# Kernel optimization log

Measured on AMD Instinct MI355X. Metric: run time of the kernel, lower is better.

## Reference

```python
import jax, jax.numpy as jnp
import numpy as np

B, C, T, V, K, O = 16, 256, 128, 64, 8, 256


def conv1x1(x, w, b):
    # x: [B,C,T,V], w: [O,C], b: [O] -> [B,O,T,V]
    return jnp.einsum('bctv,oc->botv', x, w) + b[None, :, None, None]


def batchnorm(x, gamma, beta, eps=1e-5):
    # training-mode BatchNorm2d: stats over (B,T,V) per channel
    mean = x.mean(axis=(0, 2, 3), keepdims=True)
    var = x.var(axis=(0, 2, 3), keepdims=True)
    return gamma[None, :, None, None] * (x - mean) * jax.lax.rsqrt(var + eps) + beta[None, :, None, None]


def setup_inputs() -> dict:
    key = jax.random.key(0)
    ks = jax.random.split(key, 16)
    inp = {
        'x': jax.random.normal(ks[0], (B, C, T, V), jnp.float32),
        'A_param': jax.random.normal(ks[1], (1, K, 1, V, V), jnp.float32) * 0.1,
        'alpha': jax.random.normal(ks[2], (), jnp.float32) * 0.1,
        'beta': jax.random.normal(ks[3], (), jnp.float32) * 0.1,
        'w1': jax.random.normal(ks[4], (O, C), jnp.float32) * 0.02,
        'b1': jax.random.normal(ks[5], (O,), jnp.float32) * 0.02,
        'w2': jax.random.normal(ks[6], (O, C), jnp.float32) * 0.02,
        'b2': jax.random.normal(ks[7], (O,), jnp.float32) * 0.02,
        'stem_w': jax.random.normal(ks[8], (O, C), jnp.float32) * 0.02,
        'stem_b': jax.random.normal(ks[9], (O,), jnp.float32) * 0.02,
        'stem_gamma': jnp.ones((O,), jnp.float32),
        'stem_beta': jnp.zeros((O,), jnp.float32),
        'head_w': jax.random.normal(ks[10], (O, O), jnp.float32) * 0.02,
        'head_b': jax.random.normal(ks[11], (O,), jnp.float32) * 0.02,
        'head_gamma': jnp.ones((O,), jnp.float32),
        'head_beta': jnp.zeros((O,), jnp.float32),
    }
    return inp


def reference(x, A_param, alpha, beta, w1, b1, w2, b2,
              stem_w, stem_b, stem_gamma, stem_beta,
              head_w, head_b, head_gamma, head_beta):
    b_, c_, t_, v_ = x.shape
    k_ = A_param.shape[1]
    tp = x.mean(axis=2, keepdims=True)                      # [B,C,1,V]
    x1 = conv1x1(tp, w1, b1).reshape(b_, k_, -1, v_)        # [B,K,c,V]
    x2 = conv1x1(tp, w2, b2).reshape(b_, k_, -1, v_)
    ctr = jnp.tanh(x1[..., :, None] - x2[..., None, :])     # [B,K,c,V,V]
    ada = jax.nn.softmax(jnp.einsum('bkcv,bkcw->bkvw', x1, x2)[:, :, None], axis=-2)  # [B,K,1,V,V]
    A = A_param + ctr * alpha + ada * beta                  # [B,K,c,V,V]
    res = x                                                 # in_channels == out_channels -> Identity
    h = jax.nn.relu(batchnorm(conv1x1(x, stem_w, stem_b), stem_gamma, stem_beta))
    h = h.reshape(b_, k_, -1, t_, v_)                       # [B,K,c,T,V]
    h = jnp.einsum('bkctv,bkcvw->bkctw', h, A).reshape(b_, -1, t_, v_)
    return jax.nn.relu(batchnorm(conv1x1(h, head_w, head_b), head_gamma, head_beta) + res)
```

## Files before the change

kernel.cpp:

```cpp
#include <hip/hip_runtime.h>
#include <cstdint>
#include <cstddef>

#define B_ 16
#define C_ 256
#define T_ 128
#define V_ 64
#define K_ 8
#define O_ 256
#define TN 8192
#define NBT 131072
#define NSL 32

typedef unsigned short ushort_t;
typedef __attribute__((ext_vector_type(8))) short short8;
typedef __attribute__((ext_vector_type(4))) float f32x4;

#define OFF_TP     0
#define OFF_X1     262144
#define OFF_X2     524288
#define OFF_STATS  786432
#define OFF_SSC    819200
#define OFF_HSC    819712
#define OFF_ADA    820224
#define OFF_Z      1344512
#define OFF_H2     34867200

__device__ inline ushort_t f2bf(float f) {
    unsigned u = __builtin_bit_cast(unsigned, f);
    unsigned r = (u + 0x7FFFu + ((u >> 16) & 1u)) >> 16;
    return (ushort_t)r;
}
__device__ inline unsigned pack2(float a, float b) {
    return (unsigned)f2bf(a) | ((unsigned)f2bf(b) << 16);
}
__device__ inline float bf2f_lo(unsigned u) { return __builtin_bit_cast(float, u << 16); }
__device__ inline float bf2f_hi(unsigned u) { return __builtin_bit_cast(float, u & 0xFFFF0000u); }
__device__ inline void gload_lds16(const void* g, void* l) {
    __builtin_amdgcn_global_load_lds((const __attribute__((address_space(1))) unsigned int*)g,
                                     (__attribute__((address_space(3))) unsigned int*)l, 16, 0, 0);
}

__global__ __launch_bounds__(256) void k_xpose2(const float* __restrict__ x,
                                                ushort_t* __restrict__ img,
                                                float* __restrict__ tp) {
    __shared__ float Lt[64][65];
    int tb = blockIdx.x;
    int cg = blockIdx.y;
    int b  = blockIdx.z;
    int tid = threadIdx.x;
    int c0 = cg * 64;
    float4 macc[4] = {};
    for (int tt = 0; tt < 16; tt++) {
        int t = tb * 16 + tt;
        #pragma unroll
        for (int i = 0; i < 4; i++) {
            int e = tid + i * 256;
            int ci = e >> 4, v4 = e & 15;
            float4 v = *(const float4*)(x + ((size_t)(b * C_ + c0 + ci) * 128 + t) * 64 + v4 * 4);
            *(float4*)&Lt[ci][v4 * 4] = v;
            macc[i].x += v.x; macc[i].y += v.y; macc[i].z += v.z; macc[i].w += v.w;
        }
        __syncthreads();
        #pragma unroll
        for (int i = 0; i < 2; i++) {
            int p = tid + i * 256;
            int v = p & 63, qq = (p >> 6) & 3, cc2 = p >> 8;
            int cl0 = cc2 * 32 + qq * 8;
            uint4 u;
            u.x = pack2(Lt[cl0 + 0][v], Lt[cl0 + 1][v]);
            u.y = pack2(Lt[cl0 + 2][v], Lt[cl0 + 3][v]);
            u.z = pack2(Lt[cl0 + 4][v], Lt[cl0 + 5][v]);
            u.w = pack2(Lt[cl0 + 6][v], Lt[cl0 + 7][v]);
            int cc = cg * 2 + cc2;
            size_t dst = ((size_t)(b * 128 + t) * 8 + cc) * 2048 + qq * 512 + v * 8;
            *(uint4*)(img + dst) = u;
        }
        __syncthreads();
    }
    const float r = 1.0f / (float)T_;
    #pragma unroll
    for (int i = 0; i < 4; i++) {
        int e = tid + i * 256;
        int ci = e >> 4, v4 = e & 15;
        float* dst = tp + (size_t)(b * C_ + c0 + ci) * V_ + v4 * 4;
        atomicAdd(&dst[0], macc[i].x * r); atomicAdd(&dst[1], macc[i].y * r);
        atomicAdd(&dst[2], macc[i].z * r); atomicAdd(&dst[3], macc[i].w * r);
    }
}

__global__ __launch_bounds__(256) void k_x1x2a(const float* __restrict__ tp,
                                               const float* __restrict__ w1, const float* __restrict__ b1,
                                               const float* __restrict__ w2, const float* __restrict__ b2,
                                               float* __restrict__ x1, float* __restrict__ x2) {
    int og = blockIdx.x, cc = blockIdx.y, b = blockIdx.z;
    int o  = og * 16 + (threadIdx.x >> 4);
    int v4 = threadIdx.x & 15;
    const float4* ptp = (const float4*)(tp + (size_t)b * C_ * V_) + v4;
    float4 s1 = {0.f,0.f,0.f,0.f}, s2 = {0.f,0.f,0.f,0.f};
    int c0 = cc * 64;
    for (int c = c0; c < c0 + 64; c++) {
        float4 tv = ptp[c * 16];
        float wa = w1[o * C_ + c];
        float wb = w2[o * C_ + c];
        s1.x += tv.x * wa; s1.y += tv.y * wa; s1.z += tv.z * wa; s1.w += tv.w * wa;
        s2.x += tv.x * wb; s2.y += tv.y * wb; s2.z += tv.z * wb; s2.w += tv.w * wb;
    }
    if (cc == 0) {
        float bv1 = b1[o], bv2 = b2[o];
        s1.x += bv1; s1.y += bv1; s1.z += bv1; s1.w += bv1;
        s2.x += bv2; s2.y += bv2; s2.z += bv2; s2.w += bv2;
    }
    float* p1 = x1 + (size_t)(b * O_ + o) * V_ + v4 * 4;
    float* p2 = x2 + (size_t)(b * O_ + o) * V_ + v4 * 4;
    atomicAdd(&p1[0], s1.x); atomicAdd(&p1[1], s1.y); atomicAdd(&p1[2], s1.z); atomicAdd(&p1[3], s1.w);
    atomicAdd(&p2[0], s2.x); atomicAdd(&p2[1], s2.y); atomicAdd(&p2[2], s2.z); atomicAdd(&p2[3], s2.w);
}

__global__ __launch_bounds__(64) void k_ada(const float* __restrict__ x1,
                                            const float* __restrict__ x2,
                                            float* __restrict__ ada) {
    int bid = blockIdx.x;
    int w = bid & 63;
    int k = (bid >> 6) & 7;
    int b = bid >> 9;
    int v = threadIdx.x;
    const float* p1 = x1 + ((size_t)b * O_ + k * 32) * V_;
    const float* p2 = x2 + ((size_t)b * O_ + k * 32) * V_;
    float s = 0.f;
    #pragma unroll
    for (int c = 0; c < 32; c++) s += p1[c * V_ + v] * p2[c * V_ + w];
    float m = s;
    #pragma unroll
    for (int off = 32; off >= 1; off >>= 1) m = fmaxf(m, __shfl_xor(m, off, 64));
    float e = __expf(s - m);
    float sum = e;
    #pragma unroll
    for (int off = 32; off >= 1; off >>= 1) sum += __shfl_xor(sum, off, 64);
    ada[((size_t)(b * K_ + k) * V_ + v) * V_ + w] = e / sum;
}

__global__ __launch_bounds__(256) void k_wconv(const float* __restrict__ w,
                                               ushort_t* __restrict__ img) {
    int flat = blockIdx.x * 256 + threadIdx.x;
    #pragma unroll
    for (int g2 = 0; g2 < 2; g2++) {
        int gi = flat * 2 + g2;
        int cc = gi >> 10;
        int q  = (gi >> 8) & 3;
        int ol = gi & 255;
        int c0 = cc * 32 + q * 8;
        const float* src = w + (size_t)ol * C_ + c0;
        float4 f0 = *(const float4*)src;
        float4 f1 = *(const float4*)(src + 4);
        uint4 u;
        u.x = pack2(f0.x, f0.y); u.y = pack2(f0.z, f0.w);
        u.z = pack2(f1.x, f1.y); u.w = pack2(f1.z, f1.w);
        *(uint4*)(img + (size_t)gi * 8) = u;
    }
}

__global__ __launch_bounds__(256) void k_gemm(const ushort_t* __restrict__ ximg,
                                              const ushort_t* __restrict__ wimg,
                                              const float* __restrict__ bias,
                                              ushort_t* __restrict__ out,
                                              float* __restrict__ psum,
                                              float* __restrict__ psumsq) {
    __shared__ __align__(16) ushort_t sh[2048];
    int tid = threadIdx.x;
    int nblk = blockIdx.x, b = blockIdx.z;
    int wm = tid >> 6;
    int lane = tid & 63, ln = lane & 15, q = lane >> 4;
    f32x4 acc[4][4];
    #pragma unroll
    for (int mt = 0; mt < 4; mt++)
        #pragma unroll
        for (int nt = 0; nt < 4; nt++) acc[mt][nt] = (f32x4){0.f, 0.f, 0.f, 0.f};
    const ushort_t* xbase = ximg + ((size_t)(b * 128 + nblk) * 8) * 2048;
    for (int cc = 0; cc < 8; cc++) {
        gload_lds16(xbase + (size_t)cc * 2048 + wm * 512 + lane * 8, &sh[wm * 512]);
        __syncthreads();
        short8 a[4], bb[4];
        const ushort_t* wc = wimg + (size_t)cc * 8192 + q * 2048;
        #pragma unroll
        for (int mt = 0; mt < 4; mt++)
            a[mt] = *(const short8*)(wc + (wm * 64 + mt * 16 + ln) * 8);
        #pragma unroll
        for (int nt = 0; nt < 4; nt++)
            bb[nt] = *(const short8*)&sh[q * 512 + (nt * 16 + ln) * 8];
        #pragma unroll
        for (int mt = 0; mt < 4; mt++)
            #pragma unroll
            for (int nt = 0; nt < 4; nt++)
                acc[mt][nt] = __builtin_amdgcn_mfma_f32_16x16x32_bf16(a[mt], bb[nt], acc[mt][nt], 0, 0, 0);
        __syncthreads();
    }
    int n_base = nblk * 64;
    int slice = (nblk ^ (b << 3)) & (NSL - 1);
    #pragma unroll
    for (int mt = 0; mt < 4; mt++) {
        int o0 = wm * 64 + mt * 16 + q * 4;
        #pragma unroll
        for (int r = 0; r < 4; r++) {
            float bv = bias[o0 + r];
            float v0 = acc[mt][0][r] + bv, v1 = acc[mt][1][r] + bv;
            float v2 = acc[mt][2][r] + bv, v3 = acc[mt][3][r] + bv;
            ushort_t* orow = out + ((size_t)(b * O_ + o0 + r)) * TN + n_base + ln;
            orow[0] = f2bf(v0); orow[16] = f2bf(v1); orow[32] = f2bf(v2); orow[48] = f2bf(v3);
            float s  = v0 + v1 + v2 + v3;
            float sq = v0 * v0 + v1 * v1 + v2 * v2 + v3 * v3;
            #pragma unroll
            for (int off = 1; off <= 8; off <<= 1) {
                s  += __shfl_xor(s,  off, 64);
                sq += __shfl_xor(sq, off, 64);
            }
            if (ln == 0) {
                atomicAdd(&psum[slice * 256 + o0 + r],   s);
                atomicAdd(&psumsq[slice * 256 + o0 + r], sq);
            }
        }
    }
}

__global__ void k_finalize(const float* __restrict__ psum, const float* __restrict__ psumsq,
                           const float* __restrict__ gamma, const float* __restrict__ betap,
                           float* __restrict__ scale, float* __restrict__ shift) {
    int o = threadIdx.x;
    float s = 0.f, sq = 0.f;
    #pragma unroll
    for (int sl = 0; sl < NSL; sl++) {
        s  += psum[sl * 256 + o];
        sq += psumsq[sl * 256 + o];
    }
    float mean = s  * (1.0f / (float)NBT);
    float var  = sq * (1.0f / (float)NBT) - mean * mean;
    float sc = gamma[o] * rsqrtf(var + 1e-5f);
    scale[o] = sc;
    shift[o] = betap[o] - mean * sc;
}

__global__ __launch_bounds__(256) void k_einsum_mfma(const ushort_t* __restrict__ z,
                                                     const float* __restrict__ x1,
                                                     const float* __restrict__ x2,
                                                     const float* __restrict__ ada,
                                                     const float* __restrict__ A_param,
                                                     const float* __restrict__ alphap,
                                                     const float* __restrict__ betap,
                                                     const float* __restrict__ scale,
                                                     const float* __restrict__ shift,
                                                     ushort_t* __restrict__ h2img) {
    __shared__ float Coms[4096];
    __shared__ float x1s[8][64], x2s[8][64];
    __shared__ __align__(16) ushort_t stg[8192];
    int tid = threadIdx.x;
    int bid = blockIdx.x;
    int mh = bid & 1;
    int q  = (bid >> 1) & 3;
    int k  = (bid >> 3) & 7;
    int b  = bid >> 6;
    int wm = tid >> 6;
    int lane = tid & 63, ln = lane & 15, qq = lane >> 4;
    float alpha = alphap[0], beta = betap[0];

    const float* Apk = A_param + (size_t)k * 4096;
    const float* adk = ada + (size_t)(b * K_ + k) * 4096;
    #pragma unroll
    for (int i = 0; i < 4; i++) {
        int e4 = tid + i * 256;
        float4 ap = *(const float4*)(Apk + (size_t)e4 * 4);
        float4 ad = *(const float4*)(adk + (size_t)e4 * 4);
        float4 cm = {ap.x + beta * ad.x, ap.y + beta * ad.y,
                     ap.z + beta * ad.z, ap.w + beta * ad.w};
        *(float4*)&Coms[e4 * 4] = cm;
    }
    #pragma unroll
    for (int i = 0; i < 2; i++) {
        int e = tid + i * 256;
        int cl = e >> 6, v = e & 63;
        int o1 = k * 32 + q * 8 + cl;
        x1s[cl][v] = x1[((size_t)b * O_ + o1) * V_ + v];
        x2s[cl][v] = x2[((size_t)b * O_ + o1) * V_ + v];
    }
    __syncthreads();

    short8 bfrag[2][2][4];
    #pragma unroll
    for (int half = 0; half < 2; half++) {
        int cl = wm + half * 4;
        #pragma unroll
        for (int kk = 0; kk < 2; kk++) {
            float x1v[8];
            #pragma unroll
            for (int j = 0; j < 8; j++) x1v[j] = x1s[cl][kk * 32 + qq * 8 + j];
            #pragma unroll
            for (int nt = 0; nt < 4; nt++) {
                int w = nt * 16 + ln;
                float x2v = x2s[cl][w];
                float av[8];
                #pragma unroll
                for (int j = 0; j < 8; j++) {
                    int v = kk * 32 + qq * 8 + j;
                    float d = x1v[j] - x2v;
                    float ax = fabsf(d);
                    float e2 = __expf(-2.f * ax);
                    float th = copysignf((1.f - e2) / (1.f + e2), d);
                    av[j] = Coms[v * 64 + w] + alpha * th;
                }
                uint4 bp;
                bp.x = pack2(av[0], av[1]); bp.y = pack2(av[2], av[3]);
                bp.z = pack2(av[4], av[5]); bp.w = pack2(av[6], av[7]);
                bfrag[half][kk][nt] = __builtin_bit_cast(short8, bp);
            }
        }
    }

    int o1a = k * 32 + q * 8 + wm;
    int o1b = o1a + 4;
    float scv[2] = {scale[o1a], scale[o1b]};
    float shv[2] = {shift[o1a], shift[o1b]};
    const ushort_t* zr[2] = {z + ((size_t)b * O_ + o1a) * TN, z + ((size_t)b * O_ + o1b) * TN};
    size_t obase = ((size_t)(b * 128) * 8 + k) * 2048 + q * 512;

    for (int mt = mh * 4; mt < mh * 4 + 4; mt++) {
        f32x4 acc[2][4];
        #pragma unroll
        for (int half = 0; half < 2; half++)
            #pragma unroll
            for (int nt = 0; nt < 4; nt++) acc[half][nt] = (f32x4){0.f, 0.f, 0.f, 0.f};
        #pragma unroll
        for (int half = 0; half < 2; half++) {
            float s = scv[half], h = shv[half];
            #pragma unroll
            for (int kk = 0; kk < 2; kk++) {
                const ushort_t* src = zr[half] + (mt * 16 + ln) * 64 + kk * 32 + qq * 8;
                uint4 zv = *(const uint4*)src;
                float f0 = bf2f_lo(zv.x), f1 = bf2f_hi(zv.x);
                float f2 = bf2f_lo(zv.y), f3 = bf2f_hi(zv.y);
                float f4 = bf2f_lo(zv.z), f5 = bf2f_hi(zv.z);
                float f6 = bf2f_lo(zv.w), f7 = bf2f_hi(zv.w);
                uint4 hp;
                hp.x = pack2(fmaxf(f0 * s + h, 0.f), fmaxf(f1 * s + h, 0.f));
                hp.y = pack2(fmaxf(f2 * s + h, 0.f), fmaxf(f3 * s + h, 0.f));
                hp.z = pack2(fmaxf(f4 * s + h, 0.f), fmaxf(f5 * s + h, 0.f));
                hp.w = pack2(fmaxf(f6 * s + h, 0.f), fmaxf(f7 * s + h, 0.f));
                short8 hf = __builtin_bit_cast(short8, hp);
                #pragma unroll
                for (int nt = 0; nt < 4; nt++)
                    acc[half][nt] = __builtin_amdgcn_mfma_f32_16x16x32_bf16(hf, bfrag[half][kk][nt], acc[half][nt], 0, 0, 0);
            }
        }
        #pragma unroll
        for (int half = 0; half < 2; half++) {
            int cl = wm + half * 4;
            #pragma unroll
            for (int nt = 0; nt < 4; nt++)
                #pragma unroll
                for (int r = 0; r < 4; r++)
                    stg[(qq * 4 + r) * 512 + (nt * 16 + ln) * 8 + cl] = f2bf(acc[half][nt][r]);
        }
        __syncthreads();
        #pragma unroll
        for (int ii = 0; ii < 4; ii++) {
            int u = tid + ii * 256;
            int tl = u >> 6, off = u & 63;
            ((uint4*)(h2img + obase + (size_t)(mt * 16 + tl) * 16384))[off] = ((const uint4*)stg)[u];
        }
        __syncthreads();
    }
}

__global__ __launch_bounds__(256) void k_final(const ushort_t* __restrict__ ub,
                                               const float* __restrict__ x,
                                               const float* __restrict__ scale,
                                               const float* __restrict__ shift,
                                               float* __restrict__ out) {
    size_t i4 = (size_t)blockIdx.x * 256 + threadIdx.x;
    int o = (int)((i4 >> 11) & 255);
    uint2 uv = ((const uint2*)ub)[i4];
    float4 xv = ((const float4*)x)[i4];
    float sc = scale[o], sh = shift[o];
    float4 r;
    r.x = fmaxf(bf2f_lo(uv.x) * sc + sh + xv.x, 0.f);
    r.y = fmaxf(bf2f_hi(uv.x) * sc + sh + xv.y, 0.f);
    r.z = fmaxf(bf2f_lo(uv.y) * sc + sh + xv.z, 0.f);
    r.w = fmaxf(bf2f_hi(uv.y) * sc + sh + xv.w, 0.f);
    ((float4*)out)[i4] = r;
}

extern "C" void kernel_launch(void* const* d_in, const int* in_sizes, int n_in,
                              void* d_out, int out_size, void* d_ws, size_t ws_size,
                              hipStream_t stream) {
    const float* x          = (const float*)d_in[0];
    const float* A_param    = (const float*)d_in[1];
    const float* alphap     = (const float*)d_in[2];
    const float* betap      = (const float*)d_in[3];
    const float* w1         = (const float*)d_in[4];
    const float* b1         = (const float*)d_in[5];
    const float* w2         = (const float*)d_in[6];
    const float* b2         = (const float*)d_in[7];
    const float* stem_w     = (const float*)d_in[8];
    const float* stem_b     = (const float*)d_in[9];
    const float* stem_gamma = (const float*)d_in[10];
    const float* stem_beta  = (const float*)d_in[11];
    const float* head_w     = (const float*)d_in[12];
    const float* head_b     = (const float*)d_in[13];
    const float* head_gamma = (const float*)d_in[14];
    const float* head_beta  = (const float*)d_in[15];

    float* W      = (float*)d_ws;
    float* tp     = W + OFF_TP;
    float* x1b    = W + OFF_X1;
    float* x2b    = W + OFF_X2;
    float* ssum   = W + OFF_STATS;
    float* ssq    = W + OFF_STATS + NSL * 256;
    float* hsum   = W + OFF_STATS + NSL * 512;
    float* hsq    = W + OFF_STATS + NSL * 768;
    float* sscale = W + OFF_SSC;
    float* sshift = W + OFF_SSC + 256;
    float* hscale = W + OFF_HSC;
    float* hshift = W + OFF_HSC + 256;
    float* adab   = W + OFF_ADA;
    float* uout   = (float*)d_out;

    ushort_t* xTimg  = (ushort_t*)d_out;
    ushort_t* wsimg  = (ushort_t*)(W + OFF_TP);
    ushort_t* whimg  = (ushort_t*)(W + OFF_TP + 32768);
    ushort_t* zb16   = (ushort_t*)(W + OFF_Z);
    ushort_t* ub16   = zb16;
    ushort_t* h2img  = (ushort_t*)(W + OFF_H2);

    hipMemsetAsync(W, 0, (size_t)(OFF_STATS + NSL * 1024) * sizeof(float), stream);

    k_xpose2<<<dim3(8, 4, 16), 256, 0, stream>>>(x, xTimg, tp);
    k_x1x2a<<<dim3(16, 4, 16), 256, 0, stream>>>(tp, w1, b1, w2, b2, x1b, x2b);
    k_ada<<<8192, 64, 0, stream>>>(x1b, x2b, adab);
    k_wconv<<<16, 256, 0, stream>>>(stem_w, wsimg);
    k_wconv<<<16, 256, 0, stream>>>(head_w, whimg);

    k_gemm<<<dim3(128, 1, 16), 256, 0, stream>>>(xTimg, wsimg, stem_b, zb16, ssum, ssq);
    k_finalize<<<1, 256, 0, stream>>>(ssum, ssq, stem_gamma, stem_beta, sscale, sshift);

    k_einsum_mfma<<<1024, 256, 0, stream>>>(zb16, x1b, x2b, adab, A_param, alphap, betap,
                                            sscale, sshift, h2img);

    k_gemm<<<dim3(128, 1, 16), 256, 0, stream>>>(h2img, whimg, head_b, ub16, hsum, hsq);
    k_finalize<<<1, 256, 0, stream>>>(hsum, hsq, head_gamma, head_beta, hscale, hshift);
    k_final<<<32768, 256, 0, stream>>>(ub16, x, hscale, hshift, uout);
}
```

Before: 534.6 us.

## Restructure transpose kernel with register prefetch and contiguous per-channel loads

The transpose/mean kernel now uses 512-thread blocks, each covering 32 channels by 32 timesteps. Each wave loads a contiguous 8KB run for one channel straight into registers. The next channel group is prefetched while the current group is packed to bf16 and written out, and per-channel time sums are reduced with wave shuffles before the atomics. The aim is better memory-level parallelism and coalescing in this bandwidth-bound first pass. In exchange it uses more LDS (64KB per block) and more register pressure, and it issues more atomics per channel, one set per 32 timesteps.

```diff
diff --git a/kernel.cpp b/kernel.cpp
--- a/kernel.cpp
+++ b/kernel.cpp
@@ -41,51 +41,64 @@
                                      (__attribute__((address_space(3))) unsigned int*)l, 16, 0, 0);
 }
 
-__global__ __launch_bounds__(256) void k_xpose2(const float* __restrict__ x,
+__global__ __launch_bounds__(512) void k_xpose2(const float* __restrict__ x,
                                                 ushort_t* __restrict__ img,
                                                 float* __restrict__ tp) {
-    __shared__ float Lt[64][65];
-    int tb = blockIdx.x;
+    __shared__ float L[8 * 2048];
+    int tq = blockIdx.x;
     int cg = blockIdx.y;
     int b  = blockIdx.z;
-    int tid = threadIdx.x;
-    int c0 = cg * 64;
-    float4 macc[4] = {};
-    for (int tt = 0; tt < 16; tt++) {
-        int t = tb * 16 + tt;
-        #pragma unroll
-        for (int i = 0; i < 4; i++) {
-            int e = tid + i * 256;
-            int ci = e >> 4, v4 = e & 15;
-            float4 v = *(const float4*)(x + ((size_t)(b * C_ + c0 + ci) * 128 + t) * 64 + v4 * 4);
-            *(float4*)&Lt[ci][v4 * 4] = v;
-            macc[i].x += v.x; macc[i].y += v.y; macc[i].z += v.z; macc[i].w += v.w;
-        }
-        __syncthreads();
-        #pragma unroll
-        for (int i = 0; i < 2; i++) {
-            int p = tid + i * 256;
-            int v = p & 63, qq = (p >> 6) & 3, cc2 = p >> 8;
-            int cl0 = cc2 * 32 + qq * 8;
+    int tid  = threadIdx.x;
+    int wv   = tid >> 6;
+    int lane = tid & 63;
+    int t0 = tq * 32;
+
+    float4 vreg[8];
+    auto load_regs = [&](int g) {
+        int c = cg * 32 + g * 8 + wv;
+        const float* src = x + ((size_t)(b * C_ + c) * 128 + t0) * 64 + lane * 4;
+        #pragma unroll
+        for (int i = 0; i < 8; i++)
+            vreg[i] = *(const float4*)(src + i * 256);
+    };
+
+    load_regs(0);
+    for (int g = 0; g < 4; g++) {
+        float4 s4 = {0.f, 0.f, 0.f, 0.f};
+        #pragma unroll
+        for (int i = 0; i < 8; i++) {
+            *(float4*)&L[wv * 2048 + i * 256 + lane * 4] = vreg[i];
+            s4.x += vreg[i].x; s4.y += vreg[i].y;
+            s4.z += vreg[i].z; s4.w += vreg[i].w;
+        }
+        s4.x += __shfl_xor(s4.x, 16, 64); s4.y += __shfl_xor(s4.y, 16, 64);
+        s4.z += __shfl_xor(s4.z, 16, 64); s4.w += __shfl_xor(s4.w, 16, 64);
+        s4.x += __shfl_xor(s4.x, 32, 64); s4.y += __shfl_xor(s4.y, 32, 64);
+        s4.z += __shfl_xor(s4.z, 32, 64); s4.w += __shfl_xor(s4.w, 32, 64);
+        if (lane < 16) {
+            int c = cg * 32 + g * 8 + wv;
+            const float r = 1.0f / (float)T_;
+            float* dst = tp + (size_t)(b * C_ + c) * V_ + lane * 4;
+            atomicAdd(&dst[0], s4.x * r); atomicAdd(&dst[1], s4.y * r);
+            atomicAdd(&dst[2], s4.z * r); atomicAdd(&dst[3], s4.w * r);
+        }
+        __syncthreads();
+        if (g < 3) load_regs(g + 1);
+
+        int v = tid & 63, tw = tid >> 6;
+        size_t obase = ((size_t)(b * 128 + t0) * 8 + cg) * 2048 + g * 512 + (size_t)v * 8;
+        #pragma unroll
+        for (int s = 0; s < 4; s++) {
+            int tl = s * 8 + tw;
+            const float* Lp = &L[tl * 64 + v];
             uint4 u;
-            u.x = pack2(Lt[cl0 + 0][v], Lt[cl0 + 1][v]);
-            u.y = pack2(Lt[cl0 + 2][v], Lt[cl0 + 3][v]);
-            u.z = pack2(Lt[cl0 + 4][v], Lt[cl0 + 5][v]);
-            u.w = pack2(Lt[cl0 + 6][v], Lt[cl0 + 7][v]);
-            int cc = cg * 2 + cc2;
-            size_t dst = ((size_t)(b * 128 + t) * 8 + cc) * 2048 + qq * 512 + v * 8;
-            *(uint4*)(img + dst) = u;
-        }
-        __syncthreads();
-    }
-    const float r = 1.0f / (float)T_;
-    #pragma unroll
-    for (int i = 0; i < 4; i++) {
-        int e = tid + i * 256;
-        int ci = e >> 4, v4 = e & 15;
-        float* dst = tp + (size_t)(b * C_ + c0 + ci) * V_ + v4 * 4;
-        atomicAdd(&dst[0], macc[i].x * r); atomicAdd(&dst[1], macc[i].y * r);
-        atomicAdd(&dst[2], macc[i].z * r); atomicAdd(&dst[3], macc[i].w * r);
+            u.x = pack2(Lp[0 * 2048], Lp[1 * 2048]);
+            u.y = pack2(Lp[2 * 2048], Lp[3 * 2048]);
+            u.z = pack2(Lp[4 * 2048], Lp[5 * 2048]);
+            u.w = pack2(Lp[6 * 2048], Lp[7 * 2048]);
+            *(uint4*)(img + obase + (size_t)tl * 16384) = u;
+        }
+        __syncthreads();
     }
 }
 
@@ -431,7 +444,7 @@
 
     hipMemsetAsync(W, 0, (size_t)(OFF_STATS + NSL * 1024) * sizeof(float), stream);
 
-    k_xpose2<<<dim3(8, 4, 16), 256, 0, stream>>>(x, xTimg, tp);
+    k_xpose2<<<dim3(4, 8, 16), 512, 0, stream>>>(x, xTimg, tp);
     k_x1x2a<<<dim3(16, 4, 16), 256, 0, stream>>>(tp, w1, b1, w2, b2, x1b, x2b);
     k_ada<<<8192, 64, 0, stream>>>(x1b, x2b, adab);
     k_wconv<<<16, 256, 0, stream>>>(stem_w, wsimg);
```

After: 492.6 us. 7.9% less time.
